# Kernel optimization log

Measured on AMD Instinct MI355X. Metric: run time of the kernel, lower is better.

Reference implementation:

```python
import jax, jax.numpy as jnp
import numpy as np

B, S, D, H, F = 4, 2048, 1024, 16, 4096
HD = D // H
EPS = 1e-6
ROPE_BASE = 10000.0


def apply_rope(x, positions, head_dim):
    # x: [B, S, H, hd], positions: [B, S]
    fraction = 2.0 * jnp.arange(0, head_dim // 2, dtype=jnp.float32) / head_dim
    timescale = ROPE_BASE ** fraction                      # [hd/2]
    angle = positions[:, :, None, None].astype(jnp.float32) / timescale  # [B,S,1,hd/2]
    sin, cos = jnp.sin(angle), jnp.cos(angle)
    first, second = jnp.split(x, 2, axis=-1)
    return jnp.concatenate([first * cos - second * sin,
                            second * cos + first * sin], axis=-1).astype(x.dtype)


def rms_norm(x, scale):
    var = jnp.mean(jnp.square(x), axis=-1, keepdims=True)
    return (x * jax.lax.rsqrt(var + EPS)) * scale


def setup_inputs() -> dict:
    key = jax.random.key(0)
    ks = jax.random.split(key, 10)
    std = 0.02
    x = jax.random.normal(ks[0], (B, S, D), dtype=jnp.float32)
    segment_positions = jnp.broadcast_to(jnp.arange(S, dtype=jnp.int32), (B, S))
    mask = jnp.broadcast_to(jnp.tril(jnp.ones((S, S), dtype=bool))[None, None], (B, 1, S, S))
    wq = jax.random.normal(ks[1], (D, H, HD), dtype=jnp.float32) * std
    wk = jax.random.normal(ks[2], (D, H, HD), dtype=jnp.float32) * std
    wv = jax.random.normal(ks[3], (D, H, HD), dtype=jnp.float32) * std
    wo = jax.random.normal(ks[4], (H, HD, D), dtype=jnp.float32) * std
    w_gate = jax.random.normal(ks[5], (D, F), dtype=jnp.float32) * std
    w_up = jax.random.normal(ks[6], (D, F), dtype=jnp.float32) * std
    w_down = jax.random.normal(ks[7], (F, D), dtype=jnp.float32) * std
    norm1 = jnp.ones((D,), dtype=jnp.float32)
    norm2 = jnp.ones((D,), dtype=jnp.float32)
    return dict(x=x, segment_positions=segment_positions, mask=mask,
                wq=wq, wk=wk, wv=wv, wo=wo,
                w_gate=w_gate, w_up=w_up, w_down=w_down,
                norm1=norm1, norm2=norm2)


def reference(x, segment_positions, mask, wq, wk, wv, wo, w_gate, w_up, w_down, norm1, norm2):
    # --- pre-norm RoPE attention residual block ---
    h = rms_norm(x, norm1)                                  # [B,S,D]
    q = jnp.einsum('bsd,dhk->bshk', h, wq)                  # [B,S,H,hd]
    k = jnp.einsum('bsd,dhk->bshk', h, wk)
    v = jnp.einsum('bsd,dhk->bshk', h, wv)
    q = apply_rope(q, segment_positions, HD)
    k = apply_rope(k, segment_positions, HD)
    q = q / jnp.sqrt(jnp.float32(HD))
    attn = jnp.einsum('bqhd,bkhd->bhqk', q, k)              # [B,H,S,S]
    big_neg = jnp.finfo(jnp.float32).min
    attn = jnp.where(mask, attn, big_neg)
    attn = jax.nn.softmax(attn, axis=-1)
    ctx = jnp.einsum('bhqk,bkhd->bqhd', attn, v)            # [B,S,H,hd]
    x = x + jnp.einsum('bqhd,hdo->bqo', ctx, wo)            # residual
    # --- pre-norm GLU FFN residual block ---
    h = rms_norm(x, norm2)
    gated = jax.nn.gelu(h @ w_gate) * (h @ w_up)            # [B,S,F]
    x = x + gated @ w_down
    return x
```

## Files before the change

### kernel.cpp

```cpp
#include <hip/hip_runtime.h>
#include <cstdint>
#include <cstddef>

#define BQ 4
#define SQ 2048
#define DQ 1024
#define HQ 16
#define HDQ 64
#define FQ 4096
#define MROWS (BQ * SQ)

typedef __attribute__((ext_vector_type(8))) __bf16 bf16x8;
typedef __attribute__((ext_vector_type(8))) unsigned short u16x8;
typedef __attribute__((ext_vector_type(4))) float f32x4;

__device__ __forceinline__ unsigned short f2bf(float f) {
  unsigned int u = __builtin_bit_cast(unsigned int, f);
  u = (u + 0x7FFFu + ((u >> 16) & 1u)) >> 16;
  return (unsigned short)u;
}
__device__ __forceinline__ float bf2f(unsigned short h) {
  unsigned int u = ((unsigned int)h) << 16;
  return __builtin_bit_cast(float, u);
}

typedef const unsigned int __attribute__((address_space(1))) *as1_cu32;
typedef unsigned int __attribute__((address_space(3))) *as3_u32;
#define GLD16(g, l) __builtin_amdgcn_global_load_lds((as1_cu32)(const void*)(g), (as3_u32)(void*)(l), 16, 0, 0)

__global__ __launch_bounds__(256) void k_transpose_bf16(const float* __restrict__ src,
                                                        unsigned short* __restrict__ dst,
                                                        int R, int C) {
  __shared__ float tile[32][33];
  int tx = threadIdx.x & 31, ty = threadIdx.x >> 5;
  int c0 = blockIdx.x * 32, r0 = blockIdx.y * 32;
#pragma unroll
  for (int i = 0; i < 32; i += 8)
    tile[ty + i][tx] = src[(size_t)(r0 + ty + i) * C + (c0 + tx)];
  __syncthreads();
#pragma unroll
  for (int i = 0; i < 32; i += 8)
    dst[(size_t)(c0 + ty + i) * R + (r0 + tx)] = f2bf(tile[tx][ty + i]);
}

__global__ __launch_bounds__(256) void k_rmsnorm(const float* __restrict__ x,
                                                 const float* __restrict__ g,
                                                 unsigned short* __restrict__ out) {
  int row = blockIdx.x, tid = threadIdx.x;
  const float4 v = ((const float4*)(x + (size_t)row * DQ))[tid];
  float ss = v.x * v.x + v.y * v.y + v.z * v.z + v.w * v.w;
#pragma unroll
  for (int d = 32; d >= 1; d >>= 1) ss += __shfl_xor(ss, d);
  __shared__ float ws4[4];
  if ((tid & 63) == 0) ws4[tid >> 6] = ss;
  __syncthreads();
  float tot = ws4[0] + ws4[1] + ws4[2] + ws4[3];
  float r = rsqrtf(tot * (1.0f / DQ) + 1e-6f);
  const float4 gv = ((const float4*)g)[tid];
  ushort4 o;
  o.x = f2bf(v.x * r * gv.x);
  o.y = f2bf(v.y * r * gv.y);
  o.z = f2bf(v.z * r * gv.z);
  o.w = f2bf(v.w * r * gv.w);
  ((ushort4*)(out + (size_t)row * DQ))[tid] = o;
}

template <int MODE>
__global__ __launch_bounds__(256) void k_gemm_bt(const unsigned short* __restrict__ A,
                                                 const unsigned short* __restrict__ Bt,
                                                 void* __restrict__ Cp,
                                                 const float* __restrict__ Res,
                                                 int M, int N, int K) {
  __shared__ __align__(16) unsigned short As[128 * 32];
  __shared__ __align__(16) unsigned short Bs[128 * 32];
  const int tid = threadIdx.x;
  const int lane = tid & 63, w = tid >> 6;
  const int m0 = blockIdx.y * 128, n0 = blockIdx.x * 128;
  const int wm = (w >> 1) * 64, wn = (w & 1) * 64;
  const int lr = lane & 15, lg = lane >> 4;
  f32x4 acc[4][4] = {};
  for (int k0 = 0; k0 < K; k0 += 32) {
#pragma unroll
    for (int i = 0; i < 2; ++i) {
      int flat = i * 256 + tid;
      int row = flat >> 2, ch = flat & 3;
      GLD16(A + (size_t)(m0 + row) * K + k0 + ch * 8, As + (size_t)(i * 256 + w * 64) * 8);
      GLD16(Bt + (size_t)(n0 + row) * K + k0 + ch * 8, Bs + (size_t)(i * 256 + w * 64) * 8);
    }
    __syncthreads();
    bf16x8 af[4], bfr[4];
#pragma unroll
    for (int mi = 0; mi < 4; ++mi)
      af[mi] = *(const bf16x8*)(As + (wm + mi * 16 + lr) * 32 + lg * 8);
#pragma unroll
    for (int ni = 0; ni < 4; ++ni)
      bfr[ni] = *(const bf16x8*)(Bs + (wn + ni * 16 + lr) * 32 + lg * 8);
#pragma unroll
    for (int mi = 0; mi < 4; ++mi)
#pragma unroll
      for (int ni = 0; ni < 4; ++ni)
        acc[mi][ni] = __builtin_amdgcn_mfma_f32_16x16x32_bf16(af[mi], bfr[ni], acc[mi][ni], 0, 0, 0);
    __syncthreads();
  }
#pragma unroll
  for (int mi = 0; mi < 4; ++mi) {
#pragma unroll
    for (int r = 0; r < 4; ++r) {
      int gr = m0 + wm + mi * 16 + lg * 4 + r;
#pragma unroll
      for (int ni = 0; ni < 4; ++ni) {
        int gc = n0 + wn + ni * 16 + lr;
        size_t idx = (size_t)gr * N + gc;
        float v = acc[mi][ni][r];
        if (MODE == 0) {
          ((unsigned short*)Cp)[idx] = f2bf(v);
        } else if (MODE == 1) {
          ((float*)Cp)[idx] = v + Res[idx];
        } else {
          float u = bf2f(((unsigned short*)Cp)[idx]);
          float t = v + 0.044715f * v * v * v;
          float gl = 0.5f * v * (1.0f + tanhf(0.7978845608028654f * t));
          ((unsigned short*)Cp)[idx] = f2bf(gl * u);
        }
      }
    }
  }
}

__global__ __launch_bounds__(256) void k_rope(const unsigned short* __restrict__ qkv,
                                              const int* __restrict__ pos,
                                              unsigned short* __restrict__ qp,
                                              unsigned short* __restrict__ kp,
                                              unsigned short* __restrict__ vpT) {
  __shared__ unsigned short T[64 * 67];
  const float NEG_L2TS = -0.4152410118609203f;
  const float QSCALE = 0.125f * 1.4426950408889634f;
  int bh = blockIdx.y, b = bh >> 4, hh = bh & 15;
  int s0 = blockIdx.x * 64;
  int tid = threadIdx.x;
  int row = tid >> 2, q4 = tid & 3, j0 = q4 * 8;
  int gs = s0 + row;
  const unsigned short* base = qkv + ((size_t)(b * SQ + gs)) * 3072 + hh * 64;
  u16x8 q1 = *(const u16x8*)(base + j0);
  u16x8 q2 = *(const u16x8*)(base + 32 + j0);
  u16x8 k1 = *(const u16x8*)(base + 1024 + j0);
  u16x8 k2 = *(const u16x8*)(base + 1024 + 32 + j0);
  u16x8 v1 = *(const u16x8*)(base + 2048 + j0);
  u16x8 v2 = *(const u16x8*)(base + 2048 + 32 + j0);
  float fp = (float)pos[b * SQ + gs];
  u16x8 oq1, oq2, ok1, ok2;
#pragma unroll
  for (int jj = 0; jj < 8; ++jj) {
    float ang = fp * exp2f((float)(j0 + jj) * NEG_L2TS);
    float sn, cs;
    __sincosf(ang, &sn, &cs);
    float q1f = bf2f(q1[jj]), q2f = bf2f(q2[jj]);
    float k1f = bf2f(k1[jj]), k2f = bf2f(k2[jj]);
    oq1[jj] = f2bf((q1f * cs - q2f * sn) * QSCALE);
    oq2[jj] = f2bf((q2f * cs + q1f * sn) * QSCALE);
    ok1[jj] = f2bf(k1f * cs - k2f * sn);
    ok2[jj] = f2bf(k2f * cs + k1f * sn);
    T[row * 67 + j0 + jj] = v1[jj];
    T[row * 67 + 32 + j0 + jj] = v2[jj];
  }
  size_t o = ((size_t)bh * SQ + gs) * 64;
  *(u16x8*)(qp + o + j0) = oq1;
  *(u16x8*)(qp + o + 32 + j0) = oq2;
  *(u16x8*)(kp + o + j0) = ok1;
  *(u16x8*)(kp + o + 32 + j0) = ok2;
  __syncthreads();
  int hd = tid >> 2;
#pragma unroll
  for (int c2 = 0; c2 < 2; ++c2) {
    int sb = q4 * 16 + c2 * 8;
    u16x8 ov;
#pragma unroll
    for (int ii = 0; ii < 8; ++ii) ov[ii] = T[(sb + ii) * 67 + hd];
    *(u16x8*)(vpT + ((size_t)bh * 64 + hd) * SQ + s0 + sb) = ov;
  }
}

__global__ __launch_bounds__(256) void k_flash(const unsigned short* __restrict__ qp,
                                               const unsigned short* __restrict__ kp,
                                               const unsigned short* __restrict__ vpT,
                                               unsigned short* __restrict__ ctx) {
  __shared__ __align__(16) unsigned short Ks[2][64 * 64];
  __shared__ __align__(16) unsigned short Vs[2][64 * 64];
  __shared__ __align__(16) unsigned short Ps[4][16 * 64];
  int qb = 31 - (int)blockIdx.x;
  int bh = blockIdx.y, b = bh >> 4, hh = bh & 15;
  int tid = threadIdx.x, lane = tid & 63, w = tid >> 6;
  const int lr = lane & 15, lg = lane >> 4;
  const int key = lr & 7;
  size_t hoff = (size_t)bh * SQ * 64;
  const unsigned short* Q = qp + hoff;
  const unsigned short* Kg = kp + hoff;
  const unsigned short* Vh = vpT + hoff;
  int qr0 = qb * 64 + w * 16;
  bf16x8 aq0 = *(const bf16x8*)(Q + (size_t)(qr0 + lr) * 64 + lg * 8);
  bf16x8 aq1 = *(const bf16x8*)(Q + (size_t)(qr0 + lr) * 64 + 32 + lg * 8);
  f32x4 accO[4] = {};
  float mrow[4] = {-1e30f, -1e30f, -1e30f, -1e30f};
  float lrow[4] = {0.f, 0.f, 0.f, 0.f};
  int nt = qb + 1;

#define STAGE(d, t)                                                              \
  {                                                                              \
    int kv0s = (t) * 64;                                                         \
    _Pragma("unroll") for (int i = 0; i < 2; ++i) {                              \
      int flat = i * 256 + tid;                                                  \
      int srow = flat >> 3;                                                      \
      int ch = (flat & 7) ^ (srow & 7);                                          \
      GLD16(Kg + (size_t)(kv0s + srow) * 64 + ch * 8, &Ks[d][(i * 256 + w * 64) * 8]); \
      GLD16(Vh + (size_t)srow * SQ + kv0s + ch * 8, &Vs[d][(i * 256 + w * 64) * 8]);   \
    }                                                                            \
  }

  STAGE(0, 0);
  __syncthreads();
  for (int t = 0; t < nt; ++t) {
    int kv0 = t * 64;
    if (t + 1 < nt) STAGE((t + 1) & 1, t + 1);
    const unsigned short* Kc = Ks[t & 1];
    const unsigned short* Vc = Vs[t & 1];
    f32x4 sacc[4] = {};
#pragma unroll
    for (int nh = 0; nh < 4; ++nh) {
      const unsigned short* kr = Kc + (nh * 16 + lr) * 64;
      bf16x8 b0 = *(const bf16x8*)(kr + (lg ^ key) * 8);
      bf16x8 b1 = *(const bf16x8*)(kr + ((lg + 4) ^ key) * 8);
      sacc[nh] = __builtin_amdgcn_mfma_f32_16x16x32_bf16(aq0, b0, sacc[nh], 0, 0, 0);
      sacc[nh] = __builtin_amdgcn_mfma_f32_16x16x32_bf16(aq1, b1, sacc[nh], 0, 0, 0);
    }
    bool diag = (t == qb);
    float scl[4];
#pragma unroll
    for (int i = 0; i < 4; ++i) {
      float s0 = sacc[0][i], s1 = sacc[1][i], s2 = sacc[2][i], s3 = sacc[3][i];
      if (diag) {
        int gr = qr0 + lg * 4 + i;
        int c = kv0 + lr;
        if (c > gr) s0 = -1e30f;
        if (c + 16 > gr) s1 = -1e30f;
        if (c + 32 > gr) s2 = -1e30f;
        if (c + 48 > gr) s3 = -1e30f;
      }
      float mt = fmaxf(fmaxf(s0, s1), fmaxf(s2, s3));
      mt = fmaxf(mt, __shfl_xor(mt, 1));
      mt = fmaxf(mt, __shfl_xor(mt, 2));
      mt = fmaxf(mt, __shfl_xor(mt, 4));
      mt = fmaxf(mt, __shfl_xor(mt, 8));
      float mnew = fmaxf(mrow[i], mt);
      scl[i] = exp2f(mrow[i] - mnew);
      mrow[i] = mnew;
      float p0 = exp2f(s0 - mnew), p1 = exp2f(s1 - mnew);
      float p2 = exp2f(s2 - mnew), p3 = exp2f(s3 - mnew);
      lrow[i] = lrow[i] * scl[i] + (p0 + p1 + p2 + p3);
      int prow = lg * 4 + i;
      unsigned short* Pr = &Ps[w][prow * 64];
      int pk = prow & 7;
      int sub = lr >> 3, off = lr & 7;
      Pr[((0 + sub) ^ pk) * 8 + off] = f2bf(p0);
      Pr[((2 + sub) ^ pk) * 8 + off] = f2bf(p1);
      Pr[((4 + sub) ^ pk) * 8 + off] = f2bf(p2);
      Pr[((6 + sub) ^ pk) * 8 + off] = f2bf(p3);
    }
#pragma unroll
    for (int n2 = 0; n2 < 4; ++n2)
#pragma unroll
      for (int i = 0; i < 4; ++i) accO[n2][i] *= scl[i];
    bf16x8 ap0 = *(const bf16x8*)(&Ps[w][lr * 64] + (lg ^ key) * 8);
    bf16x8 ap1 = *(const bf16x8*)(&Ps[w][lr * 64] + ((lg + 4) ^ key) * 8);
#pragma unroll
    for (int n2 = 0; n2 < 4; ++n2) {
      const unsigned short* vr = Vc + (n2 * 16 + lr) * 64;
      bf16x8 bv0 = *(const bf16x8*)(vr + (lg ^ key) * 8);
      bf16x8 bv1 = *(const bf16x8*)(vr + ((lg + 4) ^ key) * 8);
      accO[n2] = __builtin_amdgcn_mfma_f32_16x16x32_bf16(ap0, bv0, accO[n2], 0, 0, 0);
      accO[n2] = __builtin_amdgcn_mfma_f32_16x16x32_bf16(ap1, bv1, accO[n2], 0, 0, 0);
    }
    __syncthreads();
  }
#pragma unroll
  for (int i = 0; i < 4; ++i) {
    float l = lrow[i];
    l += __shfl_xor(l, 1);
    l += __shfl_xor(l, 2);
    l += __shfl_xor(l, 4);
    l += __shfl_xor(l, 8);
    lrow[i] = 1.0f / l;
  }
#pragma unroll
  for (int n2 = 0; n2 < 4; ++n2)
#pragma unroll
    for (int i = 0; i < 4; ++i) {
      int gs = qr0 + lg * 4 + i;
      ctx[((size_t)b * SQ + gs) * DQ + hh * 64 + n2 * 16 + lr] = f2bf(accO[n2][i] * lrow[i]);
    }
#undef STAGE
}

extern "C" void kernel_launch(void* const* d_in, const int* in_sizes, int n_in,
                              void* d_out, int out_size, void* d_ws, size_t ws_size,
                              hipStream_t stream) {
  (void)in_sizes; (void)n_in; (void)out_size; (void)ws_size;
  const float* x   = (const float*)d_in[0];
  const int*   pos = (const int*)d_in[1];
  const float* wq  = (const float*)d_in[3];
  const float* wk  = (const float*)d_in[4];
  const float* wv  = (const float*)d_in[5];
  const float* wo  = (const float*)d_in[6];
  const float* wg  = (const float*)d_in[7];
  const float* wu  = (const float*)d_in[8];
  const float* wd  = (const float*)d_in[9];
  const float* n1  = (const float*)d_in[10];
  const float* n2v = (const float*)d_in[11];
  char* ws = (char*)d_ws;
  const size_t MB = 1024ull * 1024ull;
  unsigned short* qkvT  = (unsigned short*)(ws);
  unsigned short* woT   = (unsigned short*)(ws + 6 * MB);
  unsigned short* gateT = (unsigned short*)(ws + 8 * MB);
  unsigned short* upT   = (unsigned short*)(ws + 16 * MB);
  unsigned short* downT = (unsigned short*)(ws + 24 * MB);
  unsigned short* qkv   = (unsigned short*)(ws + 32 * MB);
  unsigned short* act   = qkv;
  unsigned short* qpb   = (unsigned short*)(ws + 80 * MB);
  unsigned short* kpb   = (unsigned short*)(ws + 96 * MB);
  unsigned short* vpT   = (unsigned short*)(ws + 112 * MB);
  unsigned short* hbuf  = (unsigned short*)(ws + 128 * MB);
  unsigned short* ctx   = hbuf;
  float*          x2    = (float*)(ws + 144 * MB);
  unsigned short* h2    = (unsigned short*)(ws + 176 * MB);
  float*          out   = (float*)d_out;

  dim3 b256(256);
  k_transpose_bf16<<<dim3(32, 32), b256, 0, stream>>>(wq, qkvT, 1024, 1024);
  k_transpose_bf16<<<dim3(32, 32), b256, 0, stream>>>(wk, qkvT + 1024 * 1024, 1024, 1024);
  k_transpose_bf16<<<dim3(32, 32), b256, 0, stream>>>(wv, qkvT + 2 * 1024 * 1024, 1024, 1024);
  k_transpose_bf16<<<dim3(32, 32), b256, 0, stream>>>(wo, woT, 1024, 1024);
  k_transpose_bf16<<<dim3(128, 32), b256, 0, stream>>>(wg, gateT, 1024, 4096);
  k_transpose_bf16<<<dim3(128, 32), b256, 0, stream>>>(wu, upT, 1024, 4096);
  k_transpose_bf16<<<dim3(32, 128), b256, 0, stream>>>(wd, downT, 4096, 1024);
  k_rmsnorm<<<MROWS, b256, 0, stream>>>(x, n1, hbuf);
  k_gemm_bt<0><<<dim3(24, 64), b256, 0, stream>>>(hbuf, qkvT, qkv, nullptr, MROWS, 3072, 1024);
  k_rope<<<dim3(32, 64), b256, 0, stream>>>(qkv, pos, qpb, kpb, vpT);
  k_flash<<<dim3(32, 64), b256, 0, stream>>>(qpb, kpb, vpT, ctx);
  k_gemm_bt<1><<<dim3(8, 64), b256, 0, stream>>>(ctx, woT, x2, x, MROWS, 1024, 1024);
  k_rmsnorm<<<MROWS, b256, 0, stream>>>(x2, n2v, h2);
  k_gemm_bt<0><<<dim3(32, 64), b256, 0, stream>>>(h2, upT, act, nullptr, MROWS, 4096, 1024);
  k_gemm_bt<2><<<dim3(32, 64), b256, 0, stream>>>(h2, gateT, act, nullptr, MROWS, 4096, 1024);
  k_gemm_bt<1><<<dim3(8, 64), b256, 0, stream>>>(act, downT, out, x2, MROWS, 1024, 4096);
}
```

Baseline: 840.5 us.

## Add 256x256-tile 8-wave GEMM kernel with interleaved staging for QKV and FFN-up

Adds a new GEMM kernel that uses 256x256 output tiles with 512 threads, double-buffered XOR-swizzled LDS tiles, and an interleaved schedule. The schedule issues each global-load stage between MFMA quarter-blocks and raises wave priority with s_setprio during the MFMA sections. It also remaps blocks through an XCD-aware swizzle. The kernel replaces the older tile GEMM for the QKV projection and the up/gate FFN projections, aiming for higher data reuse and better overlap of loads with compute. In exchange it needs more registers per thread and many barriers, and the QKV grid (384 blocks) may fill the GPU less evenly.

Result: no change. 830.4 us (-1.2%).

```diff
diff --git a/kernel.cpp b/kernel.cpp
--- a/kernel.cpp
+++ b/kernel.cpp
@@ -125,6 +125,139 @@
       }
     }
   }
+}
+
+template <int MODE>
+__global__ __launch_bounds__(512, 2) void k_gemm256(const unsigned short* __restrict__ A,
+                                                    const unsigned short* __restrict__ Bt,
+                                                    void* __restrict__ Cp,
+                                                    int M, int N, int K) {
+  __shared__ __align__(16) unsigned short Ab[2][2][128 * 64];
+  __shared__ __align__(16) unsigned short Bb[2][2][128 * 64];
+  const int tid = threadIdx.x, lane = tid & 63, w = tid >> 6;
+  const int nwg = (int)gridDim.x;
+  const int nx = N >> 8;
+  const int cpx = nwg >> 3;
+  const int bid = (int)blockIdx.x;
+  const int swz = (bid & 7) * cpx + (bid >> 3);
+  const int bx = swz % nx, by = swz / nx;
+  const int m0 = by * 256, n0 = bx * 256;
+  const int wr = (w >> 2) * 128, wc = (w & 3) * 64;
+  const int lr = lane & 15, lg = lane >> 4;
+  const int NT = K >> 6;
+  const int r0 = tid >> 3;
+  const int c0sw = (tid & 7) ^ (r0 & 7);
+  f32x4 acc[8][4] = {};
+
+#define BAR() asm volatile("s_barrier" ::: "memory")
+
+#define STG(isB, hh_, t_)                                                         \
+  do {                                                                            \
+    int tpar = (t_) & 1;                                                          \
+    int t2 = (t_) > NT - 1 ? NT - 1 : (t_);                                       \
+    const unsigned short* gb = (isB) ? Bt : A;                                    \
+    int rb = ((isB) ? n0 : m0) + (hh_) * 128;                                     \
+    unsigned short* lb =                                                          \
+        ((isB) ? &Bb[tpar][hh_][0] : &Ab[tpar][hh_][0]) + (size_t)(w * 64) * 8;   \
+    const unsigned short* g0 = gb + (size_t)(rb + r0) * K + t2 * 64 + c0sw * 8;   \
+    GLD16(g0, lb);                                                                \
+    GLD16(g0 + (size_t)64 * K, lb + 512 * 8);                                     \
+  } while (0)
+
+#define RD_A(dst, MH, par)                                                        \
+  _Pragma("unroll") for (int mi2 = 0; mi2 < 4; ++mi2) {                           \
+    int rr = (wr + ((MH)*4 + mi2) * 16 + lr) & 127;                               \
+    int hh = wr >> 7;                                                             \
+    _Pragma("unroll") for (int ks = 0; ks < 2; ++ks)                              \
+        dst[mi2][ks] =                                                            \
+        *(const bf16x8*)&Ab[par][hh][rr * 64 + (((ks * 4 + lg) ^ (rr & 7)) * 8)]; \
+  }
+
+#define RD_B(dst, NH, par)                                                        \
+  _Pragma("unroll") for (int ni2 = 0; ni2 < 2; ++ni2) {                           \
+    int c256 = wc + ((NH)*2 + ni2) * 16 + lr;                                     \
+    int hh = c256 >> 7, rr = c256 & 127;                                          \
+    _Pragma("unroll") for (int ks = 0; ks < 2; ++ks)                              \
+        dst[ni2][ks] =                                                            \
+        *(const bf16x8*)&Bb[par][hh][rr * 64 + (((ks * 4 + lg) ^ (rr & 7)) * 8)]; \
+  }
+
+#define MM(MH, NH, aqv, bqv)                                                      \
+  _Pragma("unroll") for (int mi2 = 0; mi2 < 4; ++mi2)                             \
+  _Pragma("unroll") for (int ni2 = 0; ni2 < 2; ++ni2)                             \
+  _Pragma("unroll") for (int ks = 0; ks < 2; ++ks)                                \
+      acc[(MH)*4 + mi2][(NH)*2 + ni2] = __builtin_amdgcn_mfma_f32_16x16x32_bf16(  \
+          aqv[mi2][ks], bqv[ni2][ks], acc[(MH)*4 + mi2][(NH)*2 + ni2], 0, 0, 0);
+
+  STG(0, 0, 0);
+  STG(0, 1, 0);
+  STG(1, 0, 0);
+  STG(1, 1, 0);
+  STG(1, 0, 1);
+  STG(1, 1, 1);
+  asm volatile("s_waitcnt vmcnt(4)" ::: "memory");
+  BAR();
+
+  for (int kt = 0; kt < NT; ++kt) {
+    const int p = kt & 1;
+    bf16x8 aq[4][2], bq0[2][2], bq1[2][2];
+    RD_A(aq, 0, p);
+    RD_B(bq0, 0, p);
+    STG(0, 0, kt + 1);
+    BAR();
+    __builtin_amdgcn_s_setprio(1);
+    MM(0, 0, aq, bq0);
+    __builtin_amdgcn_s_setprio(0);
+    BAR();
+    RD_B(bq1, 1, p);
+    STG(0, 1, kt + 1);
+    BAR();
+    __builtin_amdgcn_s_setprio(1);
+    MM(0, 1, aq, bq1);
+    __builtin_amdgcn_s_setprio(0);
+    BAR();
+    RD_A(aq, 1, p);
+    STG(1, 0, kt + 2);
+    BAR();
+    __builtin_amdgcn_s_setprio(1);
+    MM(1, 1, aq, bq1);
+    __builtin_amdgcn_s_setprio(0);
+    BAR();
+    STG(1, 1, kt + 2);
+    asm volatile("s_waitcnt vmcnt(4)" ::: "memory");
+    BAR();
+    __builtin_amdgcn_s_setprio(1);
+    MM(1, 0, aq, bq0);
+    __builtin_amdgcn_s_setprio(0);
+    BAR();
+  }
+  asm volatile("s_waitcnt vmcnt(0)" ::: "memory");
+#pragma unroll
+  for (int mi = 0; mi < 8; ++mi) {
+#pragma unroll
+    for (int r = 0; r < 4; ++r) {
+      int gr = m0 + wr + mi * 16 + lg * 4 + r;
+#pragma unroll
+      for (int ni = 0; ni < 4; ++ni) {
+        int gc = n0 + wc + ni * 16 + lr;
+        size_t idx = (size_t)gr * N + gc;
+        float v = acc[mi][ni][r];
+        if (MODE == 0) {
+          ((unsigned short*)Cp)[idx] = f2bf(v);
+        } else {
+          float u = bf2f(((unsigned short*)Cp)[idx]);
+          float t = v + 0.044715f * v * v * v;
+          float gl = 0.5f * v * (1.0f + tanhf(0.7978845608028654f * t));
+          ((unsigned short*)Cp)[idx] = f2bf(gl * u);
+        }
+      }
+    }
+  }
+#undef BAR
+#undef STG
+#undef RD_A
+#undef RD_B
+#undef MM
 }
 
 __global__ __launch_bounds__(256) void k_rope(const unsigned short* __restrict__ qkv,
@@ -342,12 +475,12 @@
   k_transpose_bf16<<<dim3(128, 32), b256, 0, stream>>>(wu, upT, 1024, 4096);
   k_transpose_bf16<<<dim3(32, 128), b256, 0, stream>>>(wd, downT, 4096, 1024);
   k_rmsnorm<<<MROWS, b256, 0, stream>>>(x, n1, hbuf);
-  k_gemm_bt<0><<<dim3(24, 64), b256, 0, stream>>>(hbuf, qkvT, qkv, nullptr, MROWS, 3072, 1024);
+  k_gemm256<0><<<dim3(384), dim3(512), 0, stream>>>(hbuf, qkvT, qkv, MROWS, 3072, 1024);
   k_rope<<<dim3(32, 64), b256, 0, stream>>>(qkv, pos, qpb, kpb, vpT);
   k_flash<<<dim3(32, 64), b256, 0, stream>>>(qpb, kpb, vpT, ctx);
   k_gemm_bt<1><<<dim3(8, 64), b256, 0, stream>>>(ctx, woT, x2, x, MROWS, 1024, 1024);
   k_rmsnorm<<<MROWS, b256, 0, stream>>>(x2, n2v, h2);
-  k_gemm_bt<0><<<dim3(32, 64), b256, 0, stream>>>(h2, upT, act, nullptr, MROWS, 4096, 1024);
-  k_gemm_bt<2><<<dim3(32, 64), b256, 0, stream>>>(h2, gateT, act, nullptr, MROWS, 4096, 1024);
+  k_gemm256<0><<<dim3(512), dim3(512), 0, stream>>>(h2, upT, act, MROWS, 4096, 1024);
+  k_gemm256<2><<<dim3(512), dim3(512), 0, stream>>>(h2, gateT, act, MROWS, 4096, 1024);
   k_gemm_bt<1><<<dim3(8, 64), b256, 0, stream>>>(act, downT, out, x2, MROWS, 1024, 4096);
 }
```
